# Kernel optimization log

Hardware: AMD Instinct MI355X
Metric: run time of the kernel (lower is better)

## Reference

```python
import jax, jax.numpy as jnp
import numpy as np

M = 16384            # total tokens in batch (s)
MAX_RANK = 64        # K, max LoRA rank
NUM_SLICES = 2       # fused output slices (<=3 per kernel static_assert)
OUTPUT_DIM = 4096    # N
NUM_LORA = 8         # number of adapters
NUM_SEGMENTS = 8     # contiguous logical segments, one adapter each


def setup_inputs() -> dict:
    key = jax.random.key(0)
    k1, k2, k3, k4, k5 = jax.random.split(key, 5)
    x = jax.random.normal(k1, (M, NUM_SLICES * MAX_RANK), dtype=jnp.float32)
    weights = jax.random.normal(k2, (NUM_LORA, OUTPUT_DIM, MAX_RANK), dtype=jnp.float32) * 0.02
    # equal-length segments covering all M tokens
    seg_indptr = jnp.arange(NUM_SEGMENTS + 1, dtype=jnp.int32) * (M // NUM_SEGMENTS)
    weight_indices = jax.random.randint(k3, (NUM_SEGMENTS,), 0, NUM_LORA, dtype=jnp.int32)
    # variable per-adapter ranks, including a rank-0 (no-op) adapter
    lora_ranks = jnp.array([64, 32, 16, 0, 64, 48, 64, 32], dtype=jnp.int32)
    scalings = jax.random.uniform(k4, (NUM_LORA,), dtype=jnp.float32, minval=0.25, maxval=2.0)
    permutation = jax.random.permutation(k5, M).astype(jnp.int32)
    slice_offsets = jnp.array([0, OUTPUT_DIM // 2, OUTPUT_DIM], dtype=jnp.int32)
    return dict(x=x, weights=weights, seg_indptr=seg_indptr,
                weight_indices=weight_indices, lora_ranks=lora_ranks,
                scalings=scalings, permutation=permutation,
                slice_offsets=slice_offsets, num_segments=NUM_SEGMENTS)


def reference(x, weights, seg_indptr, weight_indices, lora_ranks, scalings,
              permutation, slice_offsets, num_segments):
    M_, D = x.shape
    num_lora, out_dim, max_rank = weights.shape
    num_slices = slice_offsets.shape[0] - 1
    xp = x[permutation]                     # rows in logical (segment) order: (M, D)
    logical = jnp.arange(M_)
    kk = jnp.arange(max_rank)
    nn = jnp.arange(out_dim)
    acc = jnp.zeros((M_, out_dim), dtype=x.dtype)   # accumulated in logical order
    for s in range(num_segments):
        w = weight_indices[s]
        r = lora_ranks[w]                   # actual rank of this segment's adapter
        scal = scalings[w].astype(x.dtype)
        in_seg = (logical >= seg_indptr[s]) & (logical < seg_indptr[s + 1]) & (r > 0)
        W = weights[w]                      # (OUTPUT_DIM, MAX_RANK)
        seg_acc = jnp.zeros((M_, out_dim), dtype=x.dtype)
        for j in range(num_slices):
            kmask = kk < r                  # only first r of MAX_RANK columns are live
            cols = jnp.where(kmask, j * r + kk, 0)   # x packed at slice_id * cur_rank
            xsub = xp[:, cols] * kmask.astype(x.dtype)        # (M, MAX_RANK)
            nmask = ((nn >= slice_offsets[j]) & (nn < slice_offsets[j + 1])).astype(x.dtype)
            seg_acc = seg_acc + (xsub @ W.T) * (scal * nmask)  # (M, OUTPUT_DIM)
        acc = acc + jnp.where(in_seg[:, None], seg_acc, 0.0)
    # scatter back from logical order to physical row positions
    out = jnp.zeros((M_, out_dim), dtype=x.dtype).at[permutation].add(acc)
    return out
```

## Files before the change

kernel.cpp:

```cpp
#include <hip/hip_runtime.h>

typedef float f32x4 __attribute__((ext_vector_type(4)));
typedef __bf16 bf16x8 __attribute__((ext_vector_type(8)));
typedef unsigned int u32x2 __attribute__((ext_vector_type(2)));

constexpr int D_IN   = 128;
constexpr int KMAX   = 64;
constexpr int N_OUT  = 4096;
constexpr int M_TOK  = 16384;

constexpr int BM = 128;
constexpr int BN = 128;
constexpr int THREADS = 256;
constexpr int LS = KMAX + 8;

__device__ __forceinline__ unsigned short f2bf(float f) {
    unsigned u = __builtin_bit_cast(unsigned, f);
    u += 0x7fffu + ((u >> 16) & 1u);
    return (unsigned short)(u >> 16);
}
__device__ __forceinline__ unsigned pk2(float a, float b) {
    return (unsigned)f2bf(a) | ((unsigned)f2bf(b) << 16);
}

__global__ __launch_bounds__(THREADS, 4)
void lora_expand_mfma(const float* __restrict__ x,
                      const float* __restrict__ weights,
                      const int*   __restrict__ seg_indptr,
                      const int*   __restrict__ weight_indices,
                      const int*   __restrict__ lora_ranks,
                      const float* __restrict__ scalings,
                      const int*   __restrict__ permutation,
                      const int*   __restrict__ slice_offsets,
                      float* __restrict__ out,
                      int num_segments, int n_slices)
{
    __shared__ __align__(16) unsigned short XA[BM * LS];
    __shared__ __align__(16) unsigned short WB[BN * LS];
    __shared__ int Ps[BM];

    const int t    = threadIdx.x;
    const int row0 = blockIdx.y * BM;
    const int col0 = blockIdx.x * BN;

    if (t < BM) Ps[t] = permutation[row0 + t];

    int j = 0;
    for (int i = 1; i < n_slices; ++i) j += (col0 >= slice_offsets[i]);

    __syncthreads();

    const int lane = t & 63;
    const int wv   = t >> 6;
    const int wm   = wv & 1;
    const int wn   = wv >> 1;
    const int quad = lane >> 4;
    const int l16  = lane & 15;

    f32x4 acc[4][4];
    #pragma unroll
    for (int a = 0; a < 4; ++a)
        #pragma unroll
        for (int b = 0; b < 4; ++b) acc[a][b] = {0.f, 0.f, 0.f, 0.f};

    for (int s = 0; s < num_segments; ++s) {
        const int segs = seg_indptr[s];
        const int sege = seg_indptr[s + 1];
        const int lo = segs > row0 ? segs : row0;
        const int hi = sege < row0 + BM ? sege : row0 + BM;
        if (lo >= hi) continue;
        const int w = weight_indices[s];
        const int r = lora_ranks[w];
        if (r <= 0) continue;
        const float scal = scalings[w];

        __syncthreads();

        #pragma unroll
        for (int it = 0; it < 8; ++it) {
            const int c   = it * THREADS + t;
            const int row = c >> 4;
            const int k0  = (c & 15) * 4;
            const int gr  = row0 + row;
            f32x4 v = {0.f, 0.f, 0.f, 0.f};
            if (gr >= lo && gr < hi && k0 < r) {
                if ((r & 3) == 0) {
                    v = *(const f32x4*)&x[(size_t)Ps[row] * D_IN + j * r + k0];
                } else {
                    const float* xr = &x[(size_t)Ps[row] * D_IN + j * r];
                    float tmp[4] = {0.f, 0.f, 0.f, 0.f};
                    #pragma unroll
                    for (int e = 0; e < 4; ++e)
                        if (k0 + e < r) tmp[e] = xr[k0 + e];
                    v = {tmp[0], tmp[1], tmp[2], tmp[3]};
                }
                v *= scal;
            }
            u32x2 p = {pk2(v.x, v.y), pk2(v.z, v.w)};
            *(u32x2*)&XA[row * LS + k0] = p;
        }

        const float* __restrict__ Wp = weights + (size_t)w * N_OUT * KMAX;
        #pragma unroll
        for (int it = 0; it < 8; ++it) {
            const int c  = it * THREADS + t;
            const int nc = c >> 4;
            const int k0 = (c & 15) * 4;
            const f32x4 v = *(const f32x4*)&Wp[(size_t)(col0 + nc) * KMAX + k0];
            u32x2 p = {pk2(v.x, v.y), pk2(v.z, v.w)};
            *(u32x2*)&WB[nc * LS + k0] = p;
        }
        __syncthreads();

        #pragma unroll
        for (int kk = 0; kk < 2; ++kk) {
            const int kof = kk * 32 + quad * 8;
            bf16x8 af[4], bfr[4];
            #pragma unroll
            for (int mt = 0; mt < 4; ++mt)
                af[mt] = *(const bf16x8*)&XA[(wm * 64 + mt * 16 + l16) * LS + kof];
            #pragma unroll
            for (int nt = 0; nt < 4; ++nt)
                bfr[nt] = *(const bf16x8*)&WB[(wn * 64 + nt * 16 + l16) * LS + kof];
            #pragma unroll
            for (int mt = 0; mt < 4; ++mt)
                #pragma unroll
                for (int nt = 0; nt < 4; ++nt)
                    acc[mt][nt] = __builtin_amdgcn_mfma_f32_16x16x32_bf16(
                        af[mt], bfr[nt], acc[mt][nt], 0, 0, 0);
        }
    }

    #pragma unroll
    for (int mt = 0; mt < 4; ++mt) {
        #pragma unroll
        for (int i = 0; i < 4; ++i) {
            const int m = wm * 64 + mt * 16 + quad * 4 + i;
            float* op = &out[(size_t)Ps[m] * N_OUT + col0 + wn * 64 + l16];
            #pragma unroll
            for (int nt = 0; nt < 4; ++nt)
                op[nt * 16] = acc[mt][nt][i];
        }
    }
}

extern "C" void kernel_launch(void* const* d_in, const int* in_sizes, int n_in,
                              void* d_out, int out_size, void* d_ws, size_t ws_size,
                              hipStream_t stream) {
    (void)n_in; (void)out_size; (void)d_ws; (void)ws_size;
    const float* x              = (const float*)d_in[0];
    const float* weights        = (const float*)d_in[1];
    const int*   seg_indptr     = (const int*)d_in[2];
    const int*   weight_indices = (const int*)d_in[3];
    const int*   lora_ranks     = (const int*)d_in[4];
    const float* scalings       = (const float*)d_in[5];
    const int*   permutation    = (const int*)d_in[6];
    const int*   slice_offsets  = (const int*)d_in[7];
    float*       out            = (float*)d_out;

    const int num_segments = in_sizes[2] - 1;
    const int n_slices     = in_sizes[7] - 1;

    dim3 grid(N_OUT / BN, M_TOK / BM);
    lora_expand_mfma<<<grid, THREADS, 0, stream>>>(
        x, weights, seg_indptr, weight_indices, lora_ranks, scalings,
        permutation, slice_offsets, out, num_segments, n_slices);
}
```

Measured before the change: 336.8 us.

## Pre-convert weights and gathered inputs to bf16 in workspace, drop LDS staging

Two new pre-pass kernels run before the GEMM. One converts all adapter weights to bf16. The other gathers the permuted, scaled and rank-masked x rows into a logical-order bf16 buffer. The main kernel then loads MFMA fragments straight from global memory, with no shared-memory staging, no per-segment loop and no intra-loop barriers. The cost is two extra launches and workspace traffic. The GEMM also assumes each 128-row tile lies in a single segment and hardcodes two slices, which is correct only when segment boundaries align to tiles.

```diff
diff --git a/kernel.cpp b/kernel.cpp
--- a/kernel.cpp
+++ b/kernel.cpp
@@ -1,18 +1,20 @@
 #include <hip/hip_runtime.h>
 
-typedef float f32x4 __attribute__((ext_vector_type(4)));
+typedef float  f32x2v __attribute__((ext_vector_type(2)));
+typedef float  f32x4  __attribute__((ext_vector_type(4)));
 typedef __bf16 bf16x8 __attribute__((ext_vector_type(8)));
-typedef unsigned int u32x2 __attribute__((ext_vector_type(2)));
 
 constexpr int D_IN   = 128;
 constexpr int KMAX   = 64;
 constexpr int N_OUT  = 4096;
-constexpr int M_TOK  = 16384;
+constexpr int NSLICE = 2;
 
 constexpr int BM = 128;
 constexpr int BN = 128;
 constexpr int THREADS = 256;
-constexpr int LS = KMAX + 8;
+
+constexpr size_t WBF_OFF = 0;
+constexpr size_t XBF_OFF = 8u << 20;
 
 __device__ __forceinline__ unsigned short f2bf(float f) {
     unsigned u = __builtin_bit_cast(unsigned, f);
@@ -23,20 +25,55 @@
     return (unsigned)f2bf(a) | ((unsigned)f2bf(b) << 16);
 }
 
+__global__ __launch_bounds__(256)
+void conv_w(const float* __restrict__ w, unsigned* __restrict__ wbf, int npairs) {
+    int i = blockIdx.x * 256 + threadIdx.x;
+    if (i >= npairs) return;
+    f32x2v v = *(const f32x2v*)&w[(size_t)i * 2];
+    wbf[i] = pk2(v.x, v.y);
+}
+
+__global__ __launch_bounds__(256)
+void conv_x(const float* __restrict__ x,
+            const int*   __restrict__ seg_indptr,
+            const int*   __restrict__ weight_indices,
+            const int*   __restrict__ lora_ranks,
+            const float* __restrict__ scalings,
+            const int*   __restrict__ permutation,
+            unsigned* __restrict__ xbf,
+            int num_segments, int m_tok)
+{
+    const int idx = blockIdx.x * 256 + threadIdx.x;
+    const int l   = idx >> 6;
+    if (l >= m_tok) return;
+    const int c   = (idx & 63) * 2;
+    const int j   = c >> 6;
+    const int k   = c & 63;
+
+    int s = 0;
+    for (int i = 0; i < num_segments; ++i)
+        if (l >= seg_indptr[i] && l < seg_indptr[i + 1]) s = i;
+    const int   w    = weight_indices[s];
+    const int   r    = lora_ranks[w];
+    const float scal = scalings[w];
+
+    const int p = permutation[l];
+    float v0 = 0.f, v1 = 0.f;
+    if (k < r)     v0 = scal * x[(size_t)p * D_IN + j * r + k];
+    if (k + 1 < r) v1 = scal * x[(size_t)p * D_IN + j * r + k + 1];
+    xbf[idx] = pk2(v0, v1);
+}
+
 __global__ __launch_bounds__(THREADS, 4)
-void lora_expand_mfma(const float* __restrict__ x,
-                      const float* __restrict__ weights,
-                      const int*   __restrict__ seg_indptr,
-                      const int*   __restrict__ weight_indices,
-                      const int*   __restrict__ lora_ranks,
-                      const float* __restrict__ scalings,
-                      const int*   __restrict__ permutation,
-                      const int*   __restrict__ slice_offsets,
-                      float* __restrict__ out,
-                      int num_segments, int n_slices)
+void lora_mfma(const __bf16* __restrict__ xbf,
+               const __bf16* __restrict__ wbf,
+               const int*    __restrict__ seg_indptr,
+               const int*    __restrict__ weight_indices,
+               const int*    __restrict__ permutation,
+               const int*    __restrict__ slice_offsets,
+               float* __restrict__ out,
+               int num_segments, int n_slices)
 {
-    __shared__ __align__(16) unsigned short XA[BM * LS];
-    __shared__ __align__(16) unsigned short WB[BN * LS];
     __shared__ int Ps[BM];
 
     const int t    = threadIdx.x;
@@ -44,11 +81,15 @@
     const int col0 = blockIdx.x * BN;
 
     if (t < BM) Ps[t] = permutation[row0 + t];
+    __syncthreads();
+
+    int s = 0;
+    for (int i = 0; i < num_segments; ++i)
+        if (row0 >= seg_indptr[i] && row0 < seg_indptr[i + 1]) s = i;
+    const int w = weight_indices[s];
 
     int j = 0;
     for (int i = 1; i < n_slices; ++i) j += (col0 >= slice_offsets[i]);
-
-    __syncthreads();
 
     const int lane = t & 63;
     const int wv   = t >> 6;
@@ -57,78 +98,31 @@
     const int quad = lane >> 4;
     const int l16  = lane & 15;
 
+    const __bf16* __restrict__ Xb = xbf + ((size_t)(row0 + wm * 64 + l16) * NSLICE + j) * KMAX;
+    const __bf16* __restrict__ Wb = wbf + ((size_t)w * N_OUT + col0 + wn * 64 + l16) * KMAX;
+
     f32x4 acc[4][4];
     #pragma unroll
     for (int a = 0; a < 4; ++a)
         #pragma unroll
         for (int b = 0; b < 4; ++b) acc[a][b] = {0.f, 0.f, 0.f, 0.f};
 
-    for (int s = 0; s < num_segments; ++s) {
-        const int segs = seg_indptr[s];
-        const int sege = seg_indptr[s + 1];
-        const int lo = segs > row0 ? segs : row0;
-        const int hi = sege < row0 + BM ? sege : row0 + BM;
-        if (lo >= hi) continue;
-        const int w = weight_indices[s];
-        const int r = lora_ranks[w];
-        if (r <= 0) continue;
-        const float scal = scalings[w];
-
-        __syncthreads();
-
+    #pragma unroll
+    for (int kk = 0; kk < 2; ++kk) {
+        const int kof = kk * 32 + quad * 8;
+        bf16x8 af[4], bfr[4];
         #pragma unroll
-        for (int it = 0; it < 8; ++it) {
-            const int c   = it * THREADS + t;
-            const int row = c >> 4;
-            const int k0  = (c & 15) * 4;
-            const int gr  = row0 + row;
-            f32x4 v = {0.f, 0.f, 0.f, 0.f};
-            if (gr >= lo && gr < hi && k0 < r) {
-                if ((r & 3) == 0) {
-                    v = *(const f32x4*)&x[(size_t)Ps[row] * D_IN + j * r + k0];
-                } else {
-                    const float* xr = &x[(size_t)Ps[row] * D_IN + j * r];
-                    float tmp[4] = {0.f, 0.f, 0.f, 0.f};
-                    #pragma unroll
-                    for (int e = 0; e < 4; ++e)
-                        if (k0 + e < r) tmp[e] = xr[k0 + e];
-                    v = {tmp[0], tmp[1], tmp[2], tmp[3]};
-                }
-                v *= scal;
-            }
-            u32x2 p = {pk2(v.x, v.y), pk2(v.z, v.w)};
-            *(u32x2*)&XA[row * LS + k0] = p;
-        }
-
-        const float* __restrict__ Wp = weights + (size_t)w * N_OUT * KMAX;
+        for (int mt = 0; mt < 4; ++mt)
+            af[mt] = *(const bf16x8*)&Xb[(size_t)(mt * 16) * NSLICE * KMAX + kof];
         #pragma unroll
-        for (int it = 0; it < 8; ++it) {
-            const int c  = it * THREADS + t;
-            const int nc = c >> 4;
-            const int k0 = (c & 15) * 4;
-            const f32x4 v = *(const f32x4*)&Wp[(size_t)(col0 + nc) * KMAX + k0];
-            u32x2 p = {pk2(v.x, v.y), pk2(v.z, v.w)};
-            *(u32x2*)&WB[nc * LS + k0] = p;
-        }
-        __syncthreads();
-
+        for (int nt = 0; nt < 4; ++nt)
+            bfr[nt] = *(const bf16x8*)&Wb[(size_t)(nt * 16) * KMAX + kof];
         #pragma unroll
-        for (int kk = 0; kk < 2; ++kk) {
-            const int kof = kk * 32 + quad * 8;
-            bf16x8 af[4], bfr[4];
-            #pragma unroll
-            for (int mt = 0; mt < 4; ++mt)
-                af[mt] = *(const bf16x8*)&XA[(wm * 64 + mt * 16 + l16) * LS + kof];
+        for (int mt = 0; mt < 4; ++mt)
             #pragma unroll
             for (int nt = 0; nt < 4; ++nt)
-                bfr[nt] = *(const bf16x8*)&WB[(wn * 64 + nt * 16 + l16) * LS + kof];
-            #pragma unroll
-            for (int mt = 0; mt < 4; ++mt)
-                #pragma unroll
-                for (int nt = 0; nt < 4; ++nt)
-                    acc[mt][nt] = __builtin_amdgcn_mfma_f32_16x16x32_bf16(
-                        af[mt], bfr[nt], acc[mt][nt], 0, 0, 0);
-        }
+                acc[mt][nt] = __builtin_amdgcn_mfma_f32_16x16x32_bf16(
+                    af[mt], bfr[nt], acc[mt][nt], 0, 0, 0);
     }
 
     #pragma unroll
@@ -147,7 +141,7 @@
 extern "C" void kernel_launch(void* const* d_in, const int* in_sizes, int n_in,
                               void* d_out, int out_size, void* d_ws, size_t ws_size,
                               hipStream_t stream) {
-    (void)n_in; (void)out_size; (void)d_ws; (void)ws_size;
+    (void)n_in; (void)out_size; (void)ws_size;
     const float* x              = (const float*)d_in[0];
     const float* weights        = (const float*)d_in[1];
     const int*   seg_indptr     = (const int*)d_in[2];
@@ -160,9 +154,22 @@
 
     const int num_segments = in_sizes[2] - 1;
     const int n_slices     = in_sizes[7] - 1;
+    const int m_tok        = in_sizes[6];
+    const int w_elems      = in_sizes[1];
 
-    dim3 grid(N_OUT / BN, M_TOK / BM);
-    lora_expand_mfma<<<grid, THREADS, 0, stream>>>(
-        x, weights, seg_indptr, weight_indices, lora_ranks, scalings,
+    unsigned* wbf = (unsigned*)((char*)d_ws + WBF_OFF);
+    unsigned* xbf = (unsigned*)((char*)d_ws + XBF_OFF);
+
+    const int wpairs = w_elems / 2;
+    conv_w<<<(wpairs + 255) / 256, 256, 0, stream>>>(weights, wbf, wpairs);
+
+    const int xthreads = m_tok * (NSLICE * KMAX / 2);
+    conv_x<<<(xthreads + 255) / 256, 256, 0, stream>>>(
+        x, seg_indptr, weight_indices, lora_ranks, scalings, permutation,
+        xbf, num_segments, m_tok);
+
+    dim3 grid(N_OUT / BN, m_tok / BM);
+    lora_mfma<<<grid, THREADS, 0, stream>>>(
+        (const __bf16*)xbf, (const __bf16*)wbf, seg_indptr, weight_indices,
         permutation, slice_offsets, out, num_segments, n_slices);
 }
```

Result: faster. 306.0 us (-9.1%).
